# Kernel optimization log

Measured on AMD Instinct MI355X. Metric: run time of the kernel, lower is better.

Reference implementation:

```python
import jax, jax.numpy as jnp
import numpy as np

D_IN = 2048
D_OUT = 2048
NUM_HEADS = 16
NUM_GROUPS = 4
HEAD_DIM = D_OUT // NUM_HEADS          # 128
HEADS_PER_GROUP = NUM_HEADS // NUM_GROUPS  # 4


def setup_inputs() -> dict:
    key = jax.random.key(0)
    ks = jax.random.split(key, 6)
    b, s = 2, 2048
    x = jax.random.normal(ks[0], (b, s, D_IN), dtype=jnp.float32)
    # Store weights as [in, out] so y = x @ W (equivalent to torch Linear x @ W.T)
    sc_q = 1.0 / np.sqrt(D_IN)
    Wq = jax.random.uniform(ks[1], (D_IN, D_OUT), jnp.float32, -sc_q, sc_q)
    Wk = jax.random.uniform(ks[2], (D_IN, NUM_GROUPS * HEAD_DIM), jnp.float32, -sc_q, sc_q)
    Wv = jax.random.uniform(ks[3], (D_IN, NUM_GROUPS * HEAD_DIM), jnp.float32, -sc_q, sc_q)
    sc_o = 1.0 / np.sqrt(D_OUT)
    Wo = jax.random.uniform(ks[4], (D_OUT, D_OUT), jnp.float32, -sc_o, sc_o)
    bo = jax.random.uniform(ks[5], (D_OUT,), jnp.float32, -sc_o, sc_o)
    return {"x": x, "Wq": Wq, "Wk": Wk, "Wv": Wv, "Wo": Wo, "bo": bo}


def reference(x, Wq, Wk, Wv, Wo, bo):
    b, s, _ = x.shape
    g, hpg, hd = NUM_GROUPS, HEADS_PER_GROUP, HEAD_DIM
    # Projections; keep grouped layout instead of repeat_interleave (same math)
    q = (x @ Wq).reshape(b, s, g, hpg, hd)   # query heads ordered group-major,
                                             # matching repeat_interleave of K/V
    k = (x @ Wk).reshape(b, s, g, hd)
    v = (x @ Wv).reshape(b, s, g, hd)
    # scores: [b, g, hpg, q_len, k_len]
    scores = jnp.einsum('bqghd,bkgd->bghqk', q, k)
    causal = jnp.triu(jnp.ones((s, s), dtype=bool), k=1)  # True above diagonal
    scores = jnp.where(causal, -jnp.inf, scores)
    scale = 1.0 / jnp.sqrt(jnp.asarray(hd, dtype=scores.dtype))
    attn = jax.nn.softmax(scores * scale, axis=-1)
    ctx = jnp.einsum('bghqk,bkgd->bqghd', attn, v).reshape(b, s, D_OUT)
    return ctx @ Wo + bo
```

## Files before the change

### kernel.cpp

```cpp
#include <hip/hip_runtime.h>

typedef short v8s __attribute__((ext_vector_type(8)));
typedef float v4f __attribute__((ext_vector_type(4)));

__device__ __forceinline__ short f2bf(float f) {
  union { float f; unsigned u; } v; v.f = f;
  unsigned r = v.u + 0x7FFFu + ((v.u >> 16) & 1u);
  return (short)(r >> 16);
}

__device__ __forceinline__ void gll16(const short* g, short* l) {
  __builtin_amdgcn_global_load_lds(
      (const __attribute__((address_space(1))) void*)g,
      (__attribute__((address_space(3))) void*)l, 16, 0, 0);
}

__global__ void cast_and_transpose(const float* __restrict__ x, short* __restrict__ xb,
                                   const float* __restrict__ Wq, const float* __restrict__ Wk,
                                   const float* __restrict__ Wv, const float* __restrict__ Wo,
                                   short* __restrict__ Wqkvt, short* __restrict__ Wot) {
  const int tid = threadIdx.x;
  int bid = blockIdx.x;
  if (bid < 8192) {
    int i = bid * 256 + tid;
    float4 v = ((const float4*)x)[i];
    short4 o;
    o.x = f2bf(v.x); o.y = f2bf(v.y); o.z = f2bf(v.z); o.w = f2bf(v.w);
    ((short4*)xb)[i] = o;
    return;
  }
  __shared__ float tile[32][33];
  bid -= 8192;
  const int tx = tid & 31, ty = tid >> 5;
  int bx = bid % 160;
  const int byy = bid / 160;
  const float* src; short* dst; int C, cb; float fac = 1.0f;
  if (bx < 64)      { src = Wq; dst = Wqkvt;                        C = 2048; cb = bx;
                      fac = 0.08838834764831845f * 1.4426950408889634f; }
  else if (bx < 80) { src = Wk; dst = Wqkvt + (size_t)2048 * 2048;  C = 512;  cb = bx - 64; }
  else if (bx < 96) { src = Wv; dst = Wqkvt + (size_t)2560 * 2048;  C = 512;  cb = bx - 80; }
  else              { src = Wo; dst = Wot;                          C = 2048; cb = bx - 96; }
  const int c0 = cb * 32, r0 = byy * 32;
#pragma unroll
  for (int i = 0; i < 4; ++i)
    tile[ty + 8 * i][tx] = src[(size_t)(r0 + ty + 8 * i) * C + c0 + tx];
  __syncthreads();
#pragma unroll
  for (int i = 0; i < 4; ++i)
    dst[(size_t)(c0 + ty + 8 * i) * 2048 + r0 + tx] = f2bf(tile[tx][ty + 8 * i] * fac);
}

__global__ void transpose_v_perm(const short* __restrict__ qkv, short* __restrict__ out) {
  __shared__ short tile[32][33];
  const int tx = threadIdx.x, ty = threadIdx.y;
  const int c0 = blockIdx.x * 32, r0 = blockIdx.y * 32;
  const int z = blockIdx.z;
#pragma unroll
  for (int i = 0; i < 4; ++i)
    tile[ty + 8 * i][tx] = qkv[(size_t)(z * 2048 + r0 + ty + 8 * i) * 3072 + 2560 + c0 + tx];
  __syncthreads();
#pragma unroll
  for (int i = 0; i < 4; ++i) {
    int k = r0 + tx;
    int pk = (k & ~31) | ((((k >> 2) & 3) * 2 + ((k >> 4) & 1)) * 4) | (k & 3);
    out[(size_t)z * 512 * 2048 + (size_t)(c0 + ty + 8 * i) * 2048 + pk] = tile[tx][ty + 8 * i];
  }
}

template <int BF16_OUT>
__global__ __launch_bounds__(256, 3) void gemm_bt2p(const short* __restrict__ A,
                                                    const short* __restrict__ Bt,
                                                    void* __restrict__ Cout,
                                                    const float* __restrict__ bias,
                                                    int N, int K, int nbx, int cpx) {
  __shared__ __align__(16) short sm[2 * 8192];
  const int tid = threadIdx.x;
  const int w = tid >> 6, lane = tid & 63, quad = lane >> 4, l16 = lane & 15;
  const int wm = (w >> 1) * 64, wn = (w & 1) * 64;
  const int bid = blockIdx.x;
  const int swz = (bid & 7) * cpx + (bid >> 3);
  const int n0 = (swz % nbx) * 128, m0 = (swz / nbx) * 128;
  const int NT = K >> 5;

  const int srow = lane >> 2;
  const int sc = ((lane & 3) ^ ((lane >> 2) & 3) ^ ((lane >> 4) & 3)) * 8;
  const short* Ag = A + (size_t)(m0 + w * 16 + srow) * K + sc;
  const short* Bg = Bt + (size_t)(n0 + w * 16 + srow) * K + sc;
  short* Ad = sm + w * 512 + lane * 8;
  short* Bd = sm + 4096 + w * 512 + lane * 8;
  const size_t rjump = (size_t)64 * K;

  auto stage = [&](int t, int bf_) {
    const int k = t << 5;
    short* ad = Ad + bf_ * 8192;
    short* bd = Bd + bf_ * 8192;
    gll16(Ag + k, ad);
    gll16(Ag + k + rjump, ad + 2048);
    gll16(Bg + k, bd);
    gll16(Bg + k + rjump, bd + 2048);
  };

  const int rsc = (quad ^ (l16 & 3) ^ ((l16 >> 2) & 3)) * 8;
  const short* aBase = sm + (wm + l16) * 32 + rsc;
  const short* bBase = sm + 4096 + (wn + l16) * 32 + rsc;

  v4f acc[4][4] = {};

  stage(0, 0);
  __syncthreads();

  for (int t = 0; t < NT; ++t) {
    if (t + 1 < NT) stage(t + 1, (t + 1) & 1);
    const int bo_ = (t & 1) * 8192;
    v8s af[4], bf[4];
#pragma unroll
    for (int i = 0; i < 4; ++i) af[i] = *(const v8s*)(aBase + bo_ + i * 512);
#pragma unroll
    for (int i = 0; i < 4; ++i) bf[i] = *(const v8s*)(bBase + bo_ + i * 512);
    __builtin_amdgcn_s_setprio(1);
#pragma unroll
    for (int mi = 0; mi < 4; ++mi)
#pragma unroll
      for (int ni = 0; ni < 4; ++ni)
        acc[mi][ni] = __builtin_amdgcn_mfma_f32_16x16x32_bf16(af[mi], bf[ni], acc[mi][ni], 0, 0, 0);
    __builtin_amdgcn_s_setprio(0);
    if (t + 1 < NT) __syncthreads();
  }

#pragma unroll
  for (int mi = 0; mi < 4; ++mi) {
#pragma unroll
    for (int ni = 0; ni < 4; ++ni) {
      const int col = n0 + wn + ni * 16 + l16;
#pragma unroll
      for (int r = 0; r < 4; ++r) {
        const int row = m0 + wm + mi * 16 + quad * 4 + r;
        if (BF16_OUT) {
          ((short*)Cout)[(size_t)row * N + col] = f2bf(acc[mi][ni][r]);
        } else {
          ((float*)Cout)[(size_t)row * N + col] = acc[mi][ni][r] + bias[col];
        }
      }
    }
  }
}

__global__ __launch_bounds__(512, 2) void flash_attn8(const short* __restrict__ QKV,
                                                      const short* __restrict__ Vtb,
                                                      short* __restrict__ ctx) {
  __shared__ __align__(16) short smem[32768];
  const int tid = threadIdx.x;
  const int w = tid >> 6, lane = tid & 63, quad = lane >> 4, l16 = lane & 15;
  const int wq = w >> 1, wk = w & 1;
  const int bh = blockIdx.y;
  const int b = bh >> 4, h = bh & 15, g = h >> 2;
  v8s ones;
#pragma unroll
  for (int i = 0; i < 8; ++i) ones[i] = (short)0x3F80;

  const int krl = lane >> 4, kcl = lane & 15;
  const int vrl = lane >> 3, vcl = lane & 7;
  const short* Kg0 = QKV + (size_t)(b * 2048 + w * 8 + krl) * 3072 + 2048 + g * 128;
  const short* Vg0 = Vtb + (size_t)(b * 512 + g * 128 + w * 16 + vrl) * 2048 + (vcl ^ (vrl & 7)) * 8;
  short* kd = smem + (w * 8) * 128 + lane * 8;
  short* vd = smem + 8192 + (w * 16) * 64 + lane * 8;

  auto stage = [&](int key0, int bs) {
    const short* kg = Kg0 + (size_t)key0 * 3072;
    const short* vg = Vg0 + key0;
#pragma unroll
    for (int ii = 0; ii < 2; ++ii) {
      const int rl = (w & 1) * 8 + ii * 4 + krl;
      gll16(kg + (size_t)(ii * 4) * 3072 + (kcl ^ rl) * 8, kd + bs * 16384 + ii * 512);
      gll16(vg + (size_t)(ii * 8) * 2048, vd + bs * 16384 + ii * 512);
    }
  };

  float* red = (float*)smem;

#pragma unroll 1
  for (int half = 0; half < 2; ++half) {
    const int qt = half ? (15 - blockIdx.x) : blockIdx.x;
    const int q0 = qt * 128;
    const int qb = q0 + wq * 32;

    v8s aq[2][4];
#pragma unroll
    for (int qs = 0; qs < 2; ++qs) {
      const short* Qp = QKV + (size_t)(b * 2048 + qb + qs * 16 + l16) * 3072 + h * 128 + quad * 8;
#pragma unroll
      for (int kk = 0; kk < 4; ++kk) aq[qs][kk] = *(const v8s*)(Qp + kk * 32);
    }
    v4f o[2][8] = {};
    v4f ol[2] = {};

    __syncthreads();
    stage(0, 0);
    const int nk = 2 * qt + 2;
#pragma unroll 1
    for (int kt = 0; kt < nk; ++kt) {
      const int key0 = kt << 6;
      __syncthreads();
      if (kt + 1 < nk) stage((kt + 1) << 6, (kt + 1) & 1);
      const short* Ks = smem + (kt & 1) * 16384;
      const short* Vs = Ks + 8192;
      const int kb = key0 + wk * 32;
      if (kb > qb + 31) continue;
      v4f sf[2][2] = {};
      __builtin_amdgcn_s_setprio(1);
#pragma unroll
      for (int kfl = 0; kfl < 2; ++kfl)
#pragma unroll
        for (int kk = 0; kk < 4; ++kk) {
          v8s kfr = *(const v8s*)&Ks[((wk * 2 + kfl) * 16 + l16) * 128 + (((kk * 4 + quad) ^ l16) * 8)];
#pragma unroll
          for (int qs = 0; qs < 2; ++qs)
            sf[qs][kfl] = __builtin_amdgcn_mfma_f32_16x16x32_bf16(kfr, aq[qs][kk], sf[qs][kfl], 0, 0, 0);
        }
      __builtin_amdgcn_s_setprio(0);
      const bool diag = (kb + 31 > qb);
      v8s pa[2];
#pragma unroll
      for (int qs = 0; qs < 2; ++qs) {
        const int qg = qb + qs * 16 + l16;
        union { v8s v; unsigned u[4]; } pu;
#pragma unroll
        for (int kfl = 0; kfl < 2; ++kfl) {
          float e[4];
#pragma unroll
          for (int r = 0; r < 4; ++r) {
            float s = sf[qs][kfl][r];
            if (diag && (kb + kfl * 16 + quad * 4 + r > qg)) s = -1e30f;
            e[r] = exp2f(s);
          }
          asm("v_cvt_pk_bf16_f32 %0, %1, %2" : "=v"(pu.u[kfl * 2 + 0]) : "v"(e[0]), "v"(e[1]));
          asm("v_cvt_pk_bf16_f32 %0, %1, %2" : "=v"(pu.u[kfl * 2 + 1]) : "v"(e[2]), "v"(e[3]));
        }
        pa[qs] = pu.v;
      }
      __builtin_amdgcn_s_setprio(1);
#pragma unroll
      for (int nf = 0; nf < 8; ++nf) {
        v8s vf = *(const v8s*)&Vs[(nf * 16 + l16) * 64 + (((wk * 4 + quad) ^ (l16 & 7)) * 8)];
#pragma unroll
        for (int qs = 0; qs < 2; ++qs)
          o[qs][nf] = __builtin_amdgcn_mfma_f32_16x16x32_bf16(pa[qs], vf, o[qs][nf], 0, 0, 0);
      }
#pragma unroll
      for (int qs = 0; qs < 2; ++qs)
        ol[qs] = __builtin_amdgcn_mfma_f32_16x16x32_bf16(pa[qs], ones, ol[qs], 0, 0, 0);
      __builtin_amdgcn_s_setprio(0);
    }
    __syncthreads();

    if (wk == 1) {
#pragma unroll
      for (int qs = 0; qs < 2; ++qs)
        *(v4f*)&red[(wq * 2 + qs) * 256 + l16 * 16 + quad * 4] = ol[qs];
    }
    __syncthreads();
    if (wk == 0) {
#pragma unroll
      for (int qs = 0; qs < 2; ++qs)
        ol[qs] += *(const v4f*)&red[(wq * 2 + qs) * 256 + l16 * 16 + quad * 4];
    }
    __syncthreads();
    if (wk == 1) {
#pragma unroll
      for (int qs = 0; qs < 2; ++qs)
#pragma unroll
        for (int nf = 0; nf < 8; ++nf)
          *(v4f*)&red[(((wq * 2 + qs) * 8 + nf) * 256) + l16 * 16 + quad * 4] = o[qs][nf];
    }
    __syncthreads();
    if (wk == 0) {
#pragma unroll
      for (int qs = 0; qs < 2; ++qs) {
        float inv[4];
#pragma unroll
        for (int r = 0; r < 4; ++r) inv[r] = 1.0f / ol[qs][r];
#pragma unroll
        for (int nf = 0; nf < 8; ++nf) {
          v4f osum = o[qs][nf] + *(const v4f*)&red[(((wq * 2 + qs) * 8 + nf) * 256) + l16 * 16 + quad * 4];
#pragma unroll
          for (int r = 0; r < 4; ++r) {
            const int row = qb + qs * 16 + quad * 4 + r;
            ctx[(size_t)(b * 2048 + row) * 2048 + h * 128 + nf * 16 + l16] = f2bf(osum[r] * inv[r]);
          }
        }
      }
    }
  }
}

extern "C" void kernel_launch(void* const* d_in, const int* in_sizes, int n_in,
                              void* d_out, int out_size, void* d_ws, size_t ws_size,
                              hipStream_t stream) {
  const float* x = (const float*)d_in[0];
  const float* Wq = (const float*)d_in[1];
  const float* Wk = (const float*)d_in[2];
  const float* Wv = (const float*)d_in[3];
  const float* Wo = (const float*)d_in[4];
  const float* bo = (const float*)d_in[5];
  float* out = (float*)d_out;
  char* ws = (char*)d_ws;

  short* xb    = (short*)(ws);
  short* ctx   = (short*)(ws);
  short* Wqkvt = (short*)(ws + 16777216);
  short* Wot   = (short*)(ws + 29360128);
  short* QKV   = (short*)(ws + 37748736);
  short* Vtb   = (short*)(ws + 62914560);

  cast_and_transpose<<<18432, 256, 0, stream>>>(x, xb, Wq, Wk, Wv, Wo, Wqkvt, Wot);

  gemm_bt2p<1><<<768, 256, 0, stream>>>(xb, Wqkvt, (void*)QKV, nullptr, 3072, 2048, 24, 96);

  transpose_v_perm<<<dim3(16, 64, 2), dim3(32, 8), 0, stream>>>(QKV, Vtb);

  flash_attn8<<<dim3(8, 32), 512, 0, stream>>>(QKV, Vtb, ctx);

  gemm_bt2p<0><<<512, 256, 0, stream>>>(ctx, Wot, (void*)out, bo, 2048, 2048, 16, 64);
}
```

Before: 279.5 us.

## Triple-buffer GEMM loads and fuse V transpose into QKV GEMM epilogue

The GEMM moves from double to triple buffering in LDS, issuing loads two tiles ahead. It synchronises with explicit vmcnt waits and raw s_barrier instead of __syncthreads. The QKV projection epilogue now writes the V columns straight into the permuted transposed Vtb layout, so the separate transpose_v_perm kernel and its extra pass over V are gone. LDS per block grows to 48KB, which may limit the occupancy of three blocks per CU, and the hand-written waitcnt logic is fragile.

```diff
diff --git a/kernel.cpp b/kernel.cpp
--- a/kernel.cpp
+++ b/kernel.cpp
@@ -2,6 +2,8 @@
 
 typedef short v8s __attribute__((ext_vector_type(8)));
 typedef float v4f __attribute__((ext_vector_type(4)));
+
+#define MEMFENCE asm volatile("" ::: "memory")
 
 __device__ __forceinline__ short f2bf(float f) {
   union { float f; unsigned u; } v; v.f = f;
@@ -50,30 +52,14 @@
     dst[(size_t)(c0 + ty + 8 * i) * 2048 + r0 + tx] = f2bf(tile[tx][ty + 8 * i] * fac);
 }
 
-__global__ void transpose_v_perm(const short* __restrict__ qkv, short* __restrict__ out) {
-  __shared__ short tile[32][33];
-  const int tx = threadIdx.x, ty = threadIdx.y;
-  const int c0 = blockIdx.x * 32, r0 = blockIdx.y * 32;
-  const int z = blockIdx.z;
-#pragma unroll
-  for (int i = 0; i < 4; ++i)
-    tile[ty + 8 * i][tx] = qkv[(size_t)(z * 2048 + r0 + ty + 8 * i) * 3072 + 2560 + c0 + tx];
-  __syncthreads();
-#pragma unroll
-  for (int i = 0; i < 4; ++i) {
-    int k = r0 + tx;
-    int pk = (k & ~31) | ((((k >> 2) & 3) * 2 + ((k >> 4) & 1)) * 4) | (k & 3);
-    out[(size_t)z * 512 * 2048 + (size_t)(c0 + ty + 8 * i) * 2048 + pk] = tile[tx][ty + 8 * i];
-  }
-}
-
-template <int BF16_OUT>
-__global__ __launch_bounds__(256, 3) void gemm_bt2p(const short* __restrict__ A,
-                                                    const short* __restrict__ Bt,
-                                                    void* __restrict__ Cout,
-                                                    const float* __restrict__ bias,
-                                                    int N, int K, int nbx, int cpx) {
-  __shared__ __align__(16) short sm[2 * 8192];
+template <int MODE>
+__global__ __launch_bounds__(256, 3) void gemm_bt3(const short* __restrict__ A,
+                                                   const short* __restrict__ Bt,
+                                                   void* __restrict__ Cout,
+                                                   const float* __restrict__ bias,
+                                                   short* __restrict__ Vtb,
+                                                   int N, int K, int nbx, int cpx) {
+  __shared__ __align__(16) short sm[3 * 8192];
   const int tid = threadIdx.x;
   const int w = tid >> 6, lane = tid & 63, quad = lane >> 4, l16 = lane & 15;
   const int wm = (w >> 1) * 64, wn = (w & 1) * 64;
@@ -107,16 +93,25 @@
   v4f acc[4][4] = {};
 
   stage(0, 0);
-  __syncthreads();
-
+  stage(1, 1);
+  asm volatile("s_waitcnt vmcnt(4)" ::: "memory");
+  __builtin_amdgcn_sched_barrier(0);
+  __builtin_amdgcn_s_barrier();
+  MEMFENCE;
+
+  int bc = 0, bn = 2;
   for (int t = 0; t < NT; ++t) {
-    if (t + 1 < NT) stage(t + 1, (t + 1) & 1);
-    const int bo_ = (t & 1) * 8192;
     v8s af[4], bf[4];
-#pragma unroll
-    for (int i = 0; i < 4; ++i) af[i] = *(const v8s*)(aBase + bo_ + i * 512);
-#pragma unroll
-    for (int i = 0; i < 4; ++i) bf[i] = *(const v8s*)(bBase + bo_ + i * 512);
+    const short* ab = aBase + bc * 8192;
+    const short* bb = bBase + bc * 8192;
+#pragma unroll
+    for (int i = 0; i < 4; ++i) af[i] = *(const v8s*)(ab + i * 512);
+#pragma unroll
+    for (int i = 0; i < 4; ++i) bf[i] = *(const v8s*)(bb + i * 512);
+    if (t + 2 < NT) stage(t + 2, bn);
+    MEMFENCE;
+    __builtin_amdgcn_s_barrier();
+    MEMFENCE;
     __builtin_amdgcn_s_setprio(1);
 #pragma unroll
     for (int mi = 0; mi < 4; ++mi)
@@ -124,7 +119,15 @@
       for (int ni = 0; ni < 4; ++ni)
         acc[mi][ni] = __builtin_amdgcn_mfma_f32_16x16x32_bf16(af[mi], bf[ni], acc[mi][ni], 0, 0, 0);
     __builtin_amdgcn_s_setprio(0);
-    if (t + 1 < NT) __syncthreads();
+    if (t + 1 < NT) {
+      if (t + 2 < NT) asm volatile("s_waitcnt vmcnt(4)" ::: "memory");
+      else            asm volatile("s_waitcnt vmcnt(0)" ::: "memory");
+      __builtin_amdgcn_sched_barrier(0);
+      __builtin_amdgcn_s_barrier();
+      MEMFENCE;
+    }
+    bc = bc == 2 ? 0 : bc + 1;
+    bn = bn == 2 ? 0 : bn + 1;
   }
 
 #pragma unroll
@@ -132,13 +135,24 @@
 #pragma unroll
     for (int ni = 0; ni < 4; ++ni) {
       const int col = n0 + wn + ni * 16 + l16;
-#pragma unroll
-      for (int r = 0; r < 4; ++r) {
-        const int row = m0 + wm + mi * 16 + quad * 4 + r;
-        if (BF16_OUT) {
-          ((short*)Cout)[(size_t)row * N + col] = f2bf(acc[mi][ni][r]);
-        } else {
-          ((float*)Cout)[(size_t)row * N + col] = acc[mi][ni][r] + bias[col];
+      if (MODE == 2 && (n0 + wn + ni * 16) >= 2560) {
+        const int d = col - 2560;
+        const int row0 = m0 + wm + mi * 16 + quad * 4;
+        const int z = row0 >> 11, key0 = row0 & 2047;
+        const int pk0 = (key0 & ~31) | (((((key0 >> 2) & 3) * 2) + ((key0 >> 4) & 1)) << 2);
+        short4 s;
+        s.x = f2bf(acc[mi][ni][0]); s.y = f2bf(acc[mi][ni][1]);
+        s.z = f2bf(acc[mi][ni][2]); s.w = f2bf(acc[mi][ni][3]);
+        *(short4*)&Vtb[(size_t)z * 512 * 2048 + (size_t)d * 2048 + pk0] = s;
+      } else {
+#pragma unroll
+        for (int r = 0; r < 4; ++r) {
+          const int row = m0 + wm + mi * 16 + quad * 4 + r;
+          if (MODE == 0) {
+            ((float*)Cout)[(size_t)row * N + col] = acc[mi][ni][r] + bias[col];
+          } else {
+            ((short*)Cout)[(size_t)row * N + col] = f2bf(acc[mi][ni][r]);
+          }
         }
       }
     }
@@ -314,11 +328,9 @@
 
   cast_and_transpose<<<18432, 256, 0, stream>>>(x, xb, Wq, Wk, Wv, Wo, Wqkvt, Wot);
 
-  gemm_bt2p<1><<<768, 256, 0, stream>>>(xb, Wqkvt, (void*)QKV, nullptr, 3072, 2048, 24, 96);
-
-  transpose_v_perm<<<dim3(16, 64, 2), dim3(32, 8), 0, stream>>>(QKV, Vtb);
+  gemm_bt3<2><<<768, 256, 0, stream>>>(xb, Wqkvt, (void*)QKV, nullptr, Vtb, 3072, 2048, 24, 96);
 
   flash_attn8<<<dim3(8, 32), 512, 0, stream>>>(QKV, Vtb, ctx);
 
-  gemm_bt2p<0><<<512, 256, 0, stream>>>(ctx, Wot, (void*)out, bo, 2048, 2048, 16, 64);
-}
+  gemm_bt3<0><<<512, 256, 0, stream>>>(ctx, Wot, (void*)out, bo, nullptr, 2048, 2048, 16, 64);
+}
```

Result: no change. 280.9 us (+0.5%).

## Fuse V transpose into QKV GEMM epilogue and split attention blocks per query tile

Applied to the files above, without the earlier changes.

The QKV projection GEMM now writes the V columns straight into the transposed, key-permuted Vtb layout from its epilogue, so the separate transpose_v_perm kernel and its extra pass over V are gone. The attention kernel no longer pairs two causal query tiles per block. It launches 16x32 blocks, one query tile each, ordered heaviest first, and raises launch bounds to 4 blocks per CU. This trades the paired-tile load balancing for more parallelism and occupancy, and relies on the hardware scheduler to balance the uneven causal work.

```diff
diff --git a/kernel.cpp b/kernel.cpp
--- a/kernel.cpp
+++ b/kernel.cpp
@@ -50,28 +50,12 @@
     dst[(size_t)(c0 + ty + 8 * i) * 2048 + r0 + tx] = f2bf(tile[tx][ty + 8 * i] * fac);
 }
 
-__global__ void transpose_v_perm(const short* __restrict__ qkv, short* __restrict__ out) {
-  __shared__ short tile[32][33];
-  const int tx = threadIdx.x, ty = threadIdx.y;
-  const int c0 = blockIdx.x * 32, r0 = blockIdx.y * 32;
-  const int z = blockIdx.z;
-#pragma unroll
-  for (int i = 0; i < 4; ++i)
-    tile[ty + 8 * i][tx] = qkv[(size_t)(z * 2048 + r0 + ty + 8 * i) * 3072 + 2560 + c0 + tx];
-  __syncthreads();
-#pragma unroll
-  for (int i = 0; i < 4; ++i) {
-    int k = r0 + tx;
-    int pk = (k & ~31) | ((((k >> 2) & 3) * 2 + ((k >> 4) & 1)) * 4) | (k & 3);
-    out[(size_t)z * 512 * 2048 + (size_t)(c0 + ty + 8 * i) * 2048 + pk] = tile[tx][ty + 8 * i];
-  }
-}
-
-template <int BF16_OUT>
+template <int MODE>
 __global__ __launch_bounds__(256, 3) void gemm_bt2p(const short* __restrict__ A,
                                                     const short* __restrict__ Bt,
                                                     void* __restrict__ Cout,
                                                     const float* __restrict__ bias,
+                                                    short* __restrict__ Vtb,
                                                     int N, int K, int nbx, int cpx) {
   __shared__ __align__(16) short sm[2 * 8192];
   const int tid = threadIdx.x;
@@ -132,20 +116,31 @@
 #pragma unroll
     for (int ni = 0; ni < 4; ++ni) {
       const int col = n0 + wn + ni * 16 + l16;
-#pragma unroll
-      for (int r = 0; r < 4; ++r) {
-        const int row = m0 + wm + mi * 16 + quad * 4 + r;
-        if (BF16_OUT) {
-          ((short*)Cout)[(size_t)row * N + col] = f2bf(acc[mi][ni][r]);
-        } else {
-          ((float*)Cout)[(size_t)row * N + col] = acc[mi][ni][r] + bias[col];
+      if (MODE == 2 && (n0 + wn + ni * 16) >= 2560) {
+        const int d = col - 2560;
+        const int row0 = m0 + wm + mi * 16 + quad * 4;
+        const int z = row0 >> 11, key0 = row0 & 2047;
+        const int pk0 = (key0 & ~31) | (((((key0 >> 2) & 3) * 2) + ((key0 >> 4) & 1)) << 2);
+        short4 s;
+        s.x = f2bf(acc[mi][ni][0]); s.y = f2bf(acc[mi][ni][1]);
+        s.z = f2bf(acc[mi][ni][2]); s.w = f2bf(acc[mi][ni][3]);
+        *(short4*)&Vtb[(size_t)z * 512 * 2048 + (size_t)d * 2048 + pk0] = s;
+      } else {
+#pragma unroll
+        for (int r = 0; r < 4; ++r) {
+          const int row = m0 + wm + mi * 16 + quad * 4 + r;
+          if (MODE == 0) {
+            ((float*)Cout)[(size_t)row * N + col] = acc[mi][ni][r] + bias[col];
+          } else {
+            ((short*)Cout)[(size_t)row * N + col] = f2bf(acc[mi][ni][r]);
+          }
         }
       }
     }
   }
 }
 
-__global__ __launch_bounds__(512, 2) void flash_attn8(const short* __restrict__ QKV,
+__global__ __launch_bounds__(512, 4) void flash_attn9(const short* __restrict__ QKV,
                                                       const short* __restrict__ Vtb,
                                                       short* __restrict__ ctx) {
   __shared__ __align__(16) short smem[32768];
@@ -178,115 +173,111 @@
 
   float* red = (float*)smem;
 
+  const int qt = 15 - blockIdx.x;
+  const int q0 = qt * 128;
+  const int qb = q0 + wq * 32;
+
+  v8s aq[2][4];
+#pragma unroll
+  for (int qs = 0; qs < 2; ++qs) {
+    const short* Qp = QKV + (size_t)(b * 2048 + qb + qs * 16 + l16) * 3072 + h * 128 + quad * 8;
+#pragma unroll
+    for (int kk = 0; kk < 4; ++kk) aq[qs][kk] = *(const v8s*)(Qp + kk * 32);
+  }
+  v4f o[2][8] = {};
+  v4f ol[2] = {};
+
+  stage(0, 0);
+  const int nk = 2 * qt + 2;
 #pragma unroll 1
-  for (int half = 0; half < 2; ++half) {
-    const int qt = half ? (15 - blockIdx.x) : blockIdx.x;
-    const int q0 = qt * 128;
-    const int qb = q0 + wq * 32;
-
-    v8s aq[2][4];
+  for (int kt = 0; kt < nk; ++kt) {
+    const int key0 = kt << 6;
+    __syncthreads();
+    if (kt + 1 < nk) stage((kt + 1) << 6, (kt + 1) & 1);
+    const short* Ks = smem + (kt & 1) * 16384;
+    const short* Vs = Ks + 8192;
+    const int kb = key0 + wk * 32;
+    if (kb > qb + 31) continue;
+    v4f sf[2][2] = {};
+    __builtin_amdgcn_s_setprio(1);
+#pragma unroll
+    for (int kfl = 0; kfl < 2; ++kfl)
+#pragma unroll
+      for (int kk = 0; kk < 4; ++kk) {
+        v8s kfr = *(const v8s*)&Ks[((wk * 2 + kfl) * 16 + l16) * 128 + (((kk * 4 + quad) ^ l16) * 8)];
+#pragma unroll
+        for (int qs = 0; qs < 2; ++qs)
+          sf[qs][kfl] = __builtin_amdgcn_mfma_f32_16x16x32_bf16(kfr, aq[qs][kk], sf[qs][kfl], 0, 0, 0);
+      }
+    __builtin_amdgcn_s_setprio(0);
+    const bool diag = (kb + 31 > qb);
+    v8s pa[2];
 #pragma unroll
     for (int qs = 0; qs < 2; ++qs) {
-      const short* Qp = QKV + (size_t)(b * 2048 + qb + qs * 16 + l16) * 3072 + h * 128 + quad * 8;
-#pragma unroll
-      for (int kk = 0; kk < 4; ++kk) aq[qs][kk] = *(const v8s*)(Qp + kk * 32);
-    }
-    v4f o[2][8] = {};
-    v4f ol[2] = {};
-
-    __syncthreads();
-    stage(0, 0);
-    const int nk = 2 * qt + 2;
-#pragma unroll 1
-    for (int kt = 0; kt < nk; ++kt) {
-      const int key0 = kt << 6;
-      __syncthreads();
-      if (kt + 1 < nk) stage((kt + 1) << 6, (kt + 1) & 1);
-      const short* Ks = smem + (kt & 1) * 16384;
-      const short* Vs = Ks + 8192;
-      const int kb = key0 + wk * 32;
-      if (kb > qb + 31) continue;
-      v4f sf[2][2] = {};
-      __builtin_amdgcn_s_setprio(1);
-#pragma unroll
-      for (int kfl = 0; kfl < 2; ++kfl)
-#pragma unroll
-        for (int kk = 0; kk < 4; ++kk) {
-          v8s kfr = *(const v8s*)&Ks[((wk * 2 + kfl) * 16 + l16) * 128 + (((kk * 4 + quad) ^ l16) * 8)];
-#pragma unroll
-          for (int qs = 0; qs < 2; ++qs)
-            sf[qs][kfl] = __builtin_amdgcn_mfma_f32_16x16x32_bf16(kfr, aq[qs][kk], sf[qs][kfl], 0, 0, 0);
+      const int qg = qb + qs * 16 + l16;
+      union { v8s v; unsigned u[4]; } pu;
+#pragma unroll
+      for (int kfl = 0; kfl < 2; ++kfl) {
+        float e[4];
+#pragma unroll
+        for (int r = 0; r < 4; ++r) {
+          float s = sf[qs][kfl][r];
+          if (diag && (kb + kfl * 16 + quad * 4 + r > qg)) s = -1e30f;
+          e[r] = exp2f(s);
         }
-      __builtin_amdgcn_s_setprio(0);
-      const bool diag = (kb + 31 > qb);
-      v8s pa[2];
-#pragma unroll
-      for (int qs = 0; qs < 2; ++qs) {
-        const int qg = qb + qs * 16 + l16;
-        union { v8s v; unsigned u[4]; } pu;
-#pragma unroll
-        for (int kfl = 0; kfl < 2; ++kfl) {
-          float e[4];
-#pragma unroll
-          for (int r = 0; r < 4; ++r) {
-            float s = sf[qs][kfl][r];
-            if (diag && (kb + kfl * 16 + quad * 4 + r > qg)) s = -1e30f;
-            e[r] = exp2f(s);
-          }
-          asm("v_cvt_pk_bf16_f32 %0, %1, %2" : "=v"(pu.u[kfl * 2 + 0]) : "v"(e[0]), "v"(e[1]));
-          asm("v_cvt_pk_bf16_f32 %0, %1, %2" : "=v"(pu.u[kfl * 2 + 1]) : "v"(e[2]), "v"(e[3]));
-        }
-        pa[qs] = pu.v;
+        asm("v_cvt_pk_bf16_f32 %0, %1, %2" : "=v"(pu.u[kfl * 2 + 0]) : "v"(e[0]), "v"(e[1]));
+        asm("v_cvt_pk_bf16_f32 %0, %1, %2" : "=v"(pu.u[kfl * 2 + 1]) : "v"(e[2]), "v"(e[3]));
       }
-      __builtin_amdgcn_s_setprio(1);
+      pa[qs] = pu.v;
+    }
+    __builtin_amdgcn_s_setprio(1);
+#pragma unroll
+    for (int nf = 0; nf < 8; ++nf) {
+      v8s vf = *(const v8s*)&Vs[(nf * 16 + l16) * 64 + (((wk * 4 + quad) ^ (l16 & 7)) * 8)];
+#pragma unroll
+      for (int qs = 0; qs < 2; ++qs)
+        o[qs][nf] = __builtin_amdgcn_mfma_f32_16x16x32_bf16(pa[qs], vf, o[qs][nf], 0, 0, 0);
+    }
+#pragma unroll
+    for (int qs = 0; qs < 2; ++qs)
+      ol[qs] = __builtin_amdgcn_mfma_f32_16x16x32_bf16(pa[qs], ones, ol[qs], 0, 0, 0);
+    __builtin_amdgcn_s_setprio(0);
+  }
+  __syncthreads();
+
+  if (wk == 1) {
+#pragma unroll
+    for (int qs = 0; qs < 2; ++qs)
+      *(v4f*)&red[(wq * 2 + qs) * 256 + l16 * 16 + quad * 4] = ol[qs];
+  }
+  __syncthreads();
+  if (wk == 0) {
+#pragma unroll
+    for (int qs = 0; qs < 2; ++qs)
+      ol[qs] += *(const v4f*)&red[(wq * 2 + qs) * 256 + l16 * 16 + quad * 4];
+  }
+  __syncthreads();
+  if (wk == 1) {
+#pragma unroll
+    for (int qs = 0; qs < 2; ++qs)
+#pragma unroll
+      for (int nf = 0; nf < 8; ++nf)
+        *(v4f*)&red[(((wq * 2 + qs) * 8 + nf) * 256) + l16 * 16 + quad * 4] = o[qs][nf];
+  }
+  __syncthreads();
+  if (wk == 0) {
+#pragma unroll
+    for (int qs = 0; qs < 2; ++qs) {
+      float inv[4];
+#pragma unroll
+      for (int r = 0; r < 4; ++r) inv[r] = 1.0f / ol[qs][r];
 #pragma unroll
       for (int nf = 0; nf < 8; ++nf) {
-        v8s vf = *(const v8s*)&Vs[(nf * 16 + l16) * 64 + (((wk * 4 + quad) ^ (l16 & 7)) * 8)];
-#pragma unroll
-        for (int qs = 0; qs < 2; ++qs)
-          o[qs][nf] = __builtin_amdgcn_mfma_f32_16x16x32_bf16(pa[qs], vf, o[qs][nf], 0, 0, 0);
-      }
-#pragma unroll
-      for (int qs = 0; qs < 2; ++qs)
-        ol[qs] = __builtin_amdgcn_mfma_f32_16x16x32_bf16(pa[qs], ones, ol[qs], 0, 0, 0);
-      __builtin_amdgcn_s_setprio(0);
-    }
-    __syncthreads();
-
-    if (wk == 1) {
-#pragma unroll
-      for (int qs = 0; qs < 2; ++qs)
-        *(v4f*)&red[(wq * 2 + qs) * 256 + l16 * 16 + quad * 4] = ol[qs];
-    }
-    __syncthreads();
-    if (wk == 0) {
-#pragma unroll
-      for (int qs = 0; qs < 2; ++qs)
-        ol[qs] += *(const v4f*)&red[(wq * 2 + qs) * 256 + l16 * 16 + quad * 4];
-    }
-    __syncthreads();
-    if (wk == 1) {
-#pragma unroll
-      for (int qs = 0; qs < 2; ++qs)
-#pragma unroll
-        for (int nf = 0; nf < 8; ++nf)
-          *(v4f*)&red[(((wq * 2 + qs) * 8 + nf) * 256) + l16 * 16 + quad * 4] = o[qs][nf];
-    }
-    __syncthreads();
-    if (wk == 0) {
-#pragma unroll
-      for (int qs = 0; qs < 2; ++qs) {
-        float inv[4];
-#pragma unroll
-        for (int r = 0; r < 4; ++r) inv[r] = 1.0f / ol[qs][r];
-#pragma unroll
-        for (int nf = 0; nf < 8; ++nf) {
-          v4f osum = o[qs][nf] + *(const v4f*)&red[(((wq * 2 + qs) * 8 + nf) * 256) + l16 * 16 + quad * 4];
-#pragma unroll
-          for (int r = 0; r < 4; ++r) {
-            const int row = qb + qs * 16 + quad * 4 + r;
-            ctx[(size_t)(b * 2048 + row) * 2048 + h * 128 + nf * 16 + l16] = f2bf(osum[r] * inv[r]);
-          }
+        v4f osum = o[qs][nf] + *(const v4f*)&red[(((wq * 2 + qs) * 8 + nf) * 256) + l16 * 16 + quad * 4];
+#pragma unroll
+        for (int r = 0; r < 4; ++r) {
+          const int row = qb + qs * 16 + quad * 4 + r;
+          ctx[(size_t)(b * 2048 + row) * 2048 + h * 128 + nf * 16 + l16] = f2bf(osum[r] * inv[r]);
         }
       }
     }
@@ -314,11 +305,9 @@
 
   cast_and_transpose<<<18432, 256, 0, stream>>>(x, xb, Wq, Wk, Wv, Wo, Wqkvt, Wot);
 
-  gemm_bt2p<1><<<768, 256, 0, stream>>>(xb, Wqkvt, (void*)QKV, nullptr, 3072, 2048, 24, 96);
-
-  transpose_v_perm<<<dim3(16, 64, 2), dim3(32, 8), 0, stream>>>(QKV, Vtb);
-
-  flash_attn8<<<dim3(8, 32), 512, 0, stream>>>(QKV, Vtb, ctx);
-
-  gemm_bt2p<0><<<512, 256, 0, stream>>>(ctx, Wot, (void*)out, bo, 2048, 2048, 16, 64);
-}
+  gemm_bt2p<2><<<768, 256, 0, stream>>>(xb, Wqkvt, (void*)QKV, nullptr, Vtb, 3072, 2048, 24, 96);
+
+  flash_attn9<<<dim3(16, 32), 512, 0, stream>>>(QKV, Vtb, ctx);
+
+  gemm_bt2p<0><<<512, 256, 0, stream>>>(ctx, Wot, (void*)out, bo, nullptr, 2048, 2048, 16, 64);
+}
```

After: 530.0 us. 89.6% more time.
